# Optimization experiments

Hardware: AMD Instinct MI355X
Metric: run time of the kernel (lower is better)

## Reference

```python
import math
import jax, jax.numpy as jnp
import numpy as np

B, S, E, A, H, L, V = 4, 1024, 1024, 64, 16, 2, 32000
EPS = 1e-5
SCALE = math.sqrt(E)  # torch code scales by sqrt(input_dim) = sqrt(embedding_dim)
W_INIT_SCALE = 0.05   # torch.rand is U[0,1); scaled down for numerically sane softmax


def setup_inputs() -> dict:
    key = jax.random.key(0)
    ks = jax.random.split(key, 6)
    return {
        "x": jax.random.randint(ks[0], (B, S), 0, V),
        "emb": jax.random.normal(ks[1], (V, E), dtype=jnp.float32) * 0.02,
        "ln_gamma": jnp.ones((L, E), dtype=jnp.float32),
        "ln_beta": jnp.zeros((L, E), dtype=jnp.float32),
        "Wq": jax.random.uniform(ks[2], (L, H, A, E), dtype=jnp.float32) * W_INIT_SCALE,
        "Wk": jax.random.uniform(ks[3], (L, H, A, E), dtype=jnp.float32) * W_INIT_SCALE,
        "Wv": jax.random.uniform(ks[4], (L, H, E, E), dtype=jnp.float32) * W_INIT_SCALE,
    }


def _attn_layer(h, gamma, beta, wq, wk, wv):
    # h: [B,H,S,E]; LayerNorm over last dim (biased variance, like torch)
    mu = jnp.mean(h, axis=-1, keepdims=True)
    var = jnp.mean(jnp.square(h - mu), axis=-1, keepdims=True)
    hn = (h - mu) * jax.lax.rsqrt(var + EPS) * gamma + beta
    q = jnp.einsum('bhse,hae->bhsa', hn, wq)   # [B,H,S,A]
    k = jnp.einsum('bhse,hae->bhsa', hn, wk)   # [B,H,S,A]
    v = jnp.einsum('bhse,hoe->bhso', hn, wv)   # [B,H,S,E]
    scores = jnp.einsum('bhsa,bhta->bhst', q, k) / SCALE  # [B,H,S,S]
    w = jax.nn.softmax(scores, axis=-1)
    return jnp.einsum('bhst,bhto->bhso', w, v)  # [B,H,S,E]


def reference(x, emb, ln_gamma, ln_beta, Wq, Wk, Wv):
    # embed then replicate across heads: [B,S,E] -> [B,H,S,E]
    h = jnp.broadcast_to(emb[x][:, None, :, :], (B, H, S, E))
    for l in range(L):
        h = _attn_layer(h, ln_gamma[l], ln_beta[l], Wq[l], Wk[l], Wv[l])
    return h
```

## Files before the change

### kernel.cpp

```cpp
#include <hip/hip_runtime.h>

#define B_ 4
#define S_ 1024
#define E_ 1024
#define A_ 64
#define H_ 16
#define L_ 2

static constexpr float LN_EPS = 1e-5f;
static constexpr float INV_SCALE = 1.0f / 32.0f;

typedef __attribute__((ext_vector_type(8))) short bf16x8;
typedef __attribute__((ext_vector_type(4))) float f32x4;

__device__ __forceinline__ unsigned short f2bf(float f) {
  unsigned u = __float_as_uint(f);
  u += 0x7fffu + ((u >> 16) & 1u);
  return (unsigned short)(u >> 16);
}
__device__ __forceinline__ float bf2f(unsigned short s) {
  return __uint_as_float(((unsigned)s) << 16);
}

__device__ __forceinline__ float block_sum256(float v, float* red) {
#pragma unroll
  for (int o = 32; o > 0; o >>= 1) v += __shfl_down(v, o, 64);
  const int lane = threadIdx.x & 63;
  const int w = threadIdx.x >> 6;
  if (lane == 0) red[w] = v;
  __syncthreads();
  if (threadIdx.x == 0) red[0] = red[0] + red[1] + red[2] + red[3];
  __syncthreads();
  float r = red[0];
  __syncthreads();
  return r;
}

__global__ __launch_bounds__(256) void cvt_f32_bf16(const float* __restrict__ in,
                                                    unsigned short* __restrict__ out, long n) {
  long i = ((long)blockIdx.x * 256 + threadIdx.x) * 4;
  const long stride = (long)gridDim.x * 1024;
  for (; i < n; i += stride) {
    float4 v = *(const float4*)(in + i);
    ushort4 o;
    o.x = f2bf(v.x); o.y = f2bf(v.y); o.z = f2bf(v.z); o.w = f2bf(v.w);
    *(ushort4*)(out + i) = o;
  }
}

__global__ __launch_bounds__(256) void cvt_qk_concat(const float* __restrict__ Wq,
                                                     const float* __restrict__ Wk,
                                                     unsigned short* __restrict__ out) {
  const long total = (long)L_ * H_ * 128 * E_;
  long i = ((long)blockIdx.x * 256 + threadIdx.x) * 4;
  const long stride = (long)gridDim.x * 1024;
  for (; i < total; i += stride) {
    const long e = i % E_;
    const long rowhe = i / E_;
    const int row = (int)(rowhe % 128);
    const long lh = rowhe / 128;
    const float* src = (row < 64 ? Wq : Wk) + (lh * 64 + (row & 63)) * E_ + e;
    float4 v = *(const float4*)src;
    ushort4 o;
    o.x = f2bf(v.x); o.y = f2bf(v.y); o.z = f2bf(v.z); o.w = f2bf(v.w);
    *(ushort4*)(out + i) = o;
  }
}

__global__ __launch_bounds__(256) void embed_ln_kernel(
    const int* __restrict__ x, const float* __restrict__ emb,
    const float* __restrict__ gamma, const float* __restrict__ beta,
    unsigned short* __restrict__ out) {
  __shared__ float red[4];
  const int row = blockIdx.x;
  const int tid = threadIdx.x;
  const float* src = emb + (long)x[row] * E_;
  float4 v = *(const float4*)(src + tid * 4);
  const float mean = block_sum256(v.x + v.y + v.z + v.w, red) * (1.f / E_);
  float dx = v.x - mean, dy = v.y - mean, dz = v.z - mean, dw = v.w - mean;
  const float var = block_sum256(dx * dx + dy * dy + dz * dz + dw * dw, red) * (1.f / E_);
  const float rstd = rsqrtf(var + LN_EPS);
  float4 g = *(const float4*)(gamma + tid * 4);
  float4 b = *(const float4*)(beta + tid * 4);
  ushort4 o;
  o.x = f2bf(dx * rstd * g.x + b.x);
  o.y = f2bf(dy * rstd * g.y + b.y);
  o.z = f2bf(dz * rstd * g.z + b.z);
  o.w = f2bf(dw * rstd * g.w + b.w);
  *(ushort4*)(out + (long)row * E_ + tid * 4) = o;
}

__global__ __launch_bounds__(256) void ln_bf16_kernel(
    const unsigned short* __restrict__ h, const float* __restrict__ gamma,
    const float* __restrict__ beta, unsigned short* __restrict__ out) {
  __shared__ float red[4];
  const long row = blockIdx.x;
  const int tid = threadIdx.x;
  ushort4 raw = *(const ushort4*)(h + row * (long)E_ + tid * 4);
  float vx = bf2f(raw.x), vy = bf2f(raw.y), vz = bf2f(raw.z), vw = bf2f(raw.w);
  const float mean = block_sum256(vx + vy + vz + vw, red) * (1.f / E_);
  float dx = vx - mean, dy = vy - mean, dz = vz - mean, dw = vw - mean;
  const float var = block_sum256(dx * dx + dy * dy + dz * dz + dw * dw, red) * (1.f / E_);
  const float rstd = rsqrtf(var + LN_EPS);
  float4 g = *(const float4*)(gamma + tid * 4);
  float4 b = *(const float4*)(beta + tid * 4);
  ushort4 o;
  o.x = f2bf(dx * rstd * g.x + b.x);
  o.y = f2bf(dy * rstd * g.y + b.y);
  o.z = f2bf(dz * rstd * g.z + b.z);
  o.w = f2bf(dw * rstd * g.w + b.w);
  *(ushort4*)(out + row * E_ + tid * 4) = o;
}

__device__ __forceinline__ void gload_lds16(const void* g, void* l) {
  __builtin_amdgcn_global_load_lds((const __attribute__((address_space(1))) void*)g,
                                   (__attribute__((address_space(3))) void*)l, 16, 0, 0);
}

template <int ROWS>
__device__ __forceinline__ void stage_tile(const unsigned short* __restrict__ src, int ldRow,
                                           unsigned short* lds, int tid) {
  const int rb = tid >> 3;
  const int gslot = (tid & 7) ^ (rb & 7);
  const int wbase = (tid >> 6) * 512;
#pragma unroll
  for (int i = 0; i < ROWS / 32; ++i) {
    const unsigned short* g = src + (long)(i * 32 + rb) * ldRow + gslot * 8;
    gload_lds16(g, lds + i * 2048 + wbase);
  }
}

__device__ __forceinline__ bf16x8 lds_frag(const unsigned short* base, int r, int slot) {
  const int byteoff = (r << 7) + ((slot ^ (r & 7)) << 4);
  return *(const bf16x8*)((const char*)base + byteoff);
}

template <int BM, int BN, bool OUT_BF16>
__global__ __launch_bounds__(256) void mfma_gemm_nt(
    const unsigned short* __restrict__ Aall, const unsigned short* __restrict__ Ball,
    void* __restrict__ Call, int M, int N, int K, int lda, int ldb,
    long aSB, long aSH, long bSB, long bSH, int Hn, float alpha) {
  __shared__ unsigned short As[BM * 64];
  __shared__ unsigned short Bs[BN * 64];
  const int batch = blockIdx.z;
  const int bb = batch / Hn, hh = batch % Hn;
  const unsigned short* Ap = Aall + (long)bb * aSB + (long)hh * aSH;
  const unsigned short* Bp = Ball + (long)bb * bSB + (long)hh * bSH;
  const int tid = threadIdx.x;
  const int lane = tid & 63;
  const int wave = tid >> 6;
  const int wr = wave >> 1, wc = wave & 1;
  const int bm = blockIdx.x * BM, bn = blockIdx.y * BN;
  constexpr int FM = BM / 32, FN = BN / 32;

  f32x4 acc[FM][FN];
#pragma unroll
  for (int i = 0; i < FM; ++i)
#pragma unroll
    for (int j = 0; j < FN; ++j) acc[i][j] = (f32x4)(0.f);

  for (int k0 = 0; k0 < K; k0 += 64) {
    stage_tile<BM>(Ap + (long)bm * lda + k0, lda, As, tid);
    stage_tile<BN>(Bp + (long)bn * ldb + k0, ldb, Bs, tid);
    __syncthreads();
#pragma unroll
    for (int kb = 0; kb < 2; ++kb) {
      const int slot = (kb << 2) + (lane >> 4);
      bf16x8 af[FM], bfv[FN];
#pragma unroll
      for (int mi = 0; mi < FM; ++mi)
        af[mi] = lds_frag(As, wr * (BM / 2) + mi * 16 + (lane & 15), slot);
#pragma unroll
      for (int ni = 0; ni < FN; ++ni)
        bfv[ni] = lds_frag(Bs, wc * (BN / 2) + ni * 16 + (lane & 15), slot);
#pragma unroll
      for (int mi = 0; mi < FM; ++mi)
#pragma unroll
        for (int ni = 0; ni < FN; ++ni)
          acc[mi][ni] = __builtin_amdgcn_mfma_f32_16x16x32_bf16(af[mi], bfv[ni], acc[mi][ni], 0, 0, 0);
    }
    __syncthreads();
  }

#pragma unroll
  for (int mi = 0; mi < FM; ++mi) {
    const int row = bm + wr * (BM / 2) + mi * 16 + ((lane >> 4) << 2);
#pragma unroll
    for (int ni = 0; ni < FN; ++ni) {
      const int col = bn + wc * (BN / 2) + ni * 16 + (lane & 15);
#pragma unroll
      for (int r = 0; r < 4; ++r) {
        const float v = acc[mi][ni][r] * alpha;
        const long idx = (long)batch * M * N + (long)(row + r) * N + col;
        if constexpr (OUT_BF16)
          ((unsigned short*)Call)[idx] = f2bf(v);
        else
          ((float*)Call)[idx] = v;
      }
    }
  }
}

__device__ __forceinline__ void stage_unit256(const unsigned short* __restrict__ src, int ldRow,
                                              char* lds_unit, int tid) {
#pragma unroll
  for (int i = 0; i < 2; ++i) {
    const int r = i * 128 + (tid >> 2);
    const int sg = (tid & 3) ^ ((r >> 1) & 3);
    const unsigned short* g = src + (long)r * ldRow + sg * 8;
    gload_lds16(g, lds_unit + i * 8192 + ((tid >> 6) << 10));
  }
}

__device__ __forceinline__ bf16x8 lds_frag256(const char* opbase, int kh, int r, int ss) {
  return *(const bf16x8*)(opbase + kh * 16384 + r * 64 + ((ss ^ ((r >> 1) & 3)) << 4));
}

template <bool OUT_BF16>
__global__ __launch_bounds__(512, 2) void mfma_gemm256_nt(
    const unsigned short* __restrict__ Aall, const unsigned short* __restrict__ Ball,
    void* __restrict__ Call, int M, int N, int K, int lda, int ldb,
    long aSB, long aSH, long bSB, long bSH, int Hn, float alpha) {
  extern __shared__ char lds[];
  const int nx = gridDim.x, ny = gridDim.y;
  const int nwg = nx * ny * gridDim.z;
  int f = blockIdx.x + nx * (blockIdx.y + ny * blockIdx.z);
  if ((nwg & 7) == 0) f = (f & 7) * (nwg >> 3) + (f >> 3);
  const int bx = f % nx;
  const int by = (f / nx) % ny;
  const int batch = f / (nx * ny);

  const int bb = batch / Hn, hh = batch % Hn;
  const unsigned short* Ap = Aall + (long)bb * aSB + (long)hh * aSH + (long)bx * 256 * lda;
  const unsigned short* Bp = Ball + (long)bb * bSB + (long)hh * bSH + (long)by * 256 * ldb;
  const int tid = threadIdx.x;
  const int lane = tid & 63;
  const int w = tid >> 6;
  const int wr = w >> 2, wc = w & 3;
  const int ss = lane >> 4;
  const int ar = lane & 15;

  f32x4 acc[8][4];
#pragma unroll
  for (int i = 0; i < 8; ++i)
#pragma unroll
    for (int j = 0; j < 4; ++j) acc[i][j] = (f32x4)(0.f);

  const int NT = K >> 6;
  stage_unit256(Ap, lda, lds, tid);
  stage_unit256(Bp, ldb, lds + 32768, tid);
  stage_unit256(Ap + 32, lda, lds + 16384, tid);
  stage_unit256(Bp + 32, ldb, lds + 49152, tid);
  asm volatile("s_waitcnt vmcnt(4)\n\ts_barrier" ::: "memory");

  for (int t = 0; t < NT; ++t) {
    const char* cur = lds + (t & 1) * 65536;
    char* nxt = lds + ((t + 1) & 1) * 65536;
    const unsigned short* An = Ap + (long)(t + 1) * 64;
    const unsigned short* Bn = Bp + (long)(t + 1) * 64;
    const bool pf = (t + 1 < NT);
    bf16x8 a[4], b[4];

#pragma unroll
    for (int ni = 0; ni < 4; ++ni)
      b[ni] = lds_frag256(cur + 32768, 0, wc * 64 + ni * 16 + ar, ss);
#pragma unroll
    for (int mi = 0; mi < 4; ++mi)
      a[mi] = lds_frag256(cur, 0, wr * 128 + mi * 16 + ar, ss);
    if (pf) stage_unit256(An, lda, nxt, tid);
    asm volatile("s_barrier" ::: "memory");
    __builtin_amdgcn_s_setprio(1);
#pragma unroll
    for (int mi = 0; mi < 4; ++mi)
#pragma unroll
      for (int ni = 0; ni < 4; ++ni)
        acc[mi][ni] = __builtin_amdgcn_mfma_f32_16x16x32_bf16(a[mi], b[ni], acc[mi][ni], 0, 0, 0);
    __builtin_amdgcn_s_setprio(0);
    asm volatile("s_barrier" ::: "memory");

#pragma unroll
    for (int mi = 0; mi < 4; ++mi)
      a[mi] = lds_frag256(cur, 0, wr * 128 + 64 + mi * 16 + ar, ss);
    if (pf) stage_unit256(Bn, ldb, nxt + 32768, tid);
    if (pf) asm volatile("s_waitcnt vmcnt(4)\n\ts_barrier" ::: "memory");
    else    asm volatile("s_waitcnt vmcnt(0)\n\ts_barrier" ::: "memory");
    __builtin_amdgcn_s_setprio(1);
#pragma unroll
    for (int mi = 0; mi < 4; ++mi)
#pragma unroll
      for (int ni = 0; ni < 4; ++ni)
        acc[4 + mi][ni] = __builtin_amdgcn_mfma_f32_16x16x32_bf16(a[mi], b[ni], acc[4 + mi][ni], 0, 0, 0);
    __builtin_amdgcn_s_setprio(0);
    asm volatile("s_barrier" ::: "memory");

#pragma unroll
    for (int ni = 0; ni < 4; ++ni)
      b[ni] = lds_frag256(cur + 32768, 1, wc * 64 + ni * 16 + ar, ss);
#pragma unroll
    for (int mi = 0; mi < 4; ++mi)
      a[mi] = lds_frag256(cur, 1, wr * 128 + mi * 16 + ar, ss);
    if (pf) stage_unit256(An + 32, lda, nxt + 16384, tid);
    asm volatile("s_barrier" ::: "memory");
    __builtin_amdgcn_s_setprio(1);
#pragma unroll
    for (int mi = 0; mi < 4; ++mi)
#pragma unroll
      for (int ni = 0; ni < 4; ++ni)
        acc[mi][ni] = __builtin_amdgcn_mfma_f32_16x16x32_bf16(a[mi], b[ni], acc[mi][ni], 0, 0, 0);
    __builtin_amdgcn_s_setprio(0);
    asm volatile("s_barrier" ::: "memory");

#pragma unroll
    for (int mi = 0; mi < 4; ++mi)
      a[mi] = lds_frag256(cur, 1, wr * 128 + 64 + mi * 16 + ar, ss);
    if (pf) {
      stage_unit256(Bn + 32, ldb, nxt + 49152, tid);
      asm volatile("s_waitcnt vmcnt(4)\n\ts_barrier" ::: "memory");
    } else {
      asm volatile("s_barrier" ::: "memory");
    }
    __builtin_amdgcn_s_setprio(1);
#pragma unroll
    for (int mi = 0; mi < 4; ++mi)
#pragma unroll
      for (int ni = 0; ni < 4; ++ni)
        acc[4 + mi][ni] = __builtin_amdgcn_mfma_f32_16x16x32_bf16(a[mi], b[ni], acc[4 + mi][ni], 0, 0, 0);
    __builtin_amdgcn_s_setprio(0);
    asm volatile("s_barrier" ::: "memory");
  }

#pragma unroll
  for (int mi = 0; mi < 8; ++mi) {
    const int row0 = bx * 256 + wr * 128 + mi * 16 + ((lane >> 4) << 2);
#pragma unroll
    for (int ni = 0; ni < 4; ++ni) {
      const int col = by * 256 + wc * 64 + ni * 16 + (lane & 15);
#pragma unroll
      for (int r = 0; r < 4; ++r) {
        const float v = acc[mi][ni][r] * alpha;
        const long idx = (long)batch * M * N + (long)(row0 + r) * N + col;
        if constexpr (OUT_BF16)
          ((unsigned short*)Call)[idx] = f2bf(v);
        else
          ((float*)Call)[idx] = v;
      }
    }
  }
}

__global__ __launch_bounds__(512) void scores_softmax_kernel(
    const unsigned short* __restrict__ qk, unsigned short* __restrict__ sc) {
  extern __shared__ char smem[];
  unsigned short* q_lds = (unsigned short*)smem;
  unsigned short* k_lds = (unsigned short*)(smem + 8192);
  float* redm = (float*)(smem + 8192 + 131072);
  float* reds = redm + 512;

  const int tid = threadIdx.x;
  const int lane = tid & 63;
  const int w = tid >> 6;
  const int batch = blockIdx.z;
  const int bm = blockIdx.x * 64;
  const unsigned short* qbase = qk + (long)batch * S_ * 128 + (long)bm * 128;
  const unsigned short* kbase = qk + (long)batch * S_ * 128 + 64;

  {
    const int r = tid >> 3;
    const int slot = (tid & 7) ^ (r & 7);
    gload_lds16(qbase + (long)r * 128 + slot * 8, (char*)q_lds + w * 1024);
  }
#pragma unroll
  for (int p = 0; p < 16; ++p) {
    const int r = p * 64 + (tid >> 3);
    const int slot = (tid & 7) ^ (r & 7);
    gload_lds16(kbase + (long)r * 128 + slot * 8, (char*)k_lds + p * 8192 + w * 1024);
  }
  __syncthreads();

  const int ss = lane >> 4, ar = lane & 15;
  f32x4 acc[4][8];
#pragma unroll
  for (int i = 0; i < 4; ++i)
#pragma unroll
    for (int j = 0; j < 8; ++j) acc[i][j] = (f32x4)(0.f);

#pragma unroll
  for (int kh = 0; kh < 2; ++kh) {
    bf16x8 a[4];
#pragma unroll
    for (int mi = 0; mi < 4; ++mi)
      a[mi] = lds_frag(q_lds, mi * 16 + ar, kh * 4 + ss);
#pragma unroll
    for (int ni = 0; ni < 8; ++ni) {
      bf16x8 bv = lds_frag(k_lds, w * 128 + ni * 16 + ar, kh * 4 + ss);
#pragma unroll
      for (int mi = 0; mi < 4; ++mi)
        acc[mi][ni] = __builtin_amdgcn_mfma_f32_16x16x32_bf16(a[mi], bv, acc[mi][ni], 0, 0, 0);
    }
  }

#pragma unroll
  for (int mi = 0; mi < 4; ++mi)
#pragma unroll
    for (int ni = 0; ni < 8; ++ni)
#pragma unroll
      for (int r = 0; r < 4; ++r) acc[mi][ni][r] *= INV_SCALE;

  float gmax[4][4];
#pragma unroll
  for (int mi = 0; mi < 4; ++mi)
#pragma unroll
    for (int r = 0; r < 4; ++r) {
      float m = acc[mi][0][r];
#pragma unroll
      for (int ni = 1; ni < 8; ++ni) m = fmaxf(m, acc[mi][ni][r]);
#pragma unroll
      for (int mask = 1; mask < 16; mask <<= 1) m = fmaxf(m, __shfl_xor(m, mask, 64));
      if ((lane & 15) == 0) redm[(mi * 16 + (lane >> 4) * 4 + r) * 8 + w] = m;
      gmax[mi][r] = m;
    }
  __syncthreads();
#pragma unroll
  for (int mi = 0; mi < 4; ++mi)
#pragma unroll
    for (int r = 0; r < 4; ++r) {
      const int row = mi * 16 + (lane >> 4) * 4 + r;
      float g = redm[row * 8];
#pragma unroll
      for (int w2 = 1; w2 < 8; ++w2) g = fmaxf(g, redm[row * 8 + w2]);
      gmax[mi][r] = g;
    }

  float ginv[4][4];
#pragma unroll
  for (int mi = 0; mi < 4; ++mi)
#pragma unroll
    for (int r = 0; r < 4; ++r) {
      float s = 0.f;
#pragma unroll
      for (int ni = 0; ni < 8; ++ni) {
        const float e = __expf(acc[mi][ni][r] - gmax[mi][r]);
        acc[mi][ni][r] = e;
        s += e;
      }
#pragma unroll
      for (int mask = 1; mask < 16; mask <<= 1) s += __shfl_xor(s, mask, 64);
      if ((lane & 15) == 0) reds[(mi * 16 + (lane >> 4) * 4 + r) * 8 + w] = s;
    }
  __syncthreads();
#pragma unroll
  for (int mi = 0; mi < 4; ++mi)
#pragma unroll
    for (int r = 0; r < 4; ++r) {
      const int row = mi * 16 + (lane >> 4) * 4 + r;
      float g = 0.f;
#pragma unroll
      for (int w2 = 0; w2 < 8; ++w2) g += reds[row * 8 + w2];
      ginv[mi][r] = 1.f / g;
    }

  unsigned short* out = sc + (long)batch * S_ * S_;
#pragma unroll
  for (int mi = 0; mi < 4; ++mi)
#pragma unroll
    for (int r = 0; r < 4; ++r) {
      const long row = bm + mi * 16 + (lane >> 4) * 4 + r;
#pragma unroll
      for (int ni = 0; ni < 8; ++ni) {
        const int col = w * 128 + ni * 16 + ar;
        out[row * S_ + col] = f2bf(acc[mi][ni][r] * ginv[mi][r]);
      }
    }
}

extern "C" void kernel_launch(void* const* d_in, const int* in_sizes, int n_in,
                              void* d_out, int out_size, void* d_ws, size_t ws_size,
                              hipStream_t stream) {
  const int* x = (const int*)d_in[0];
  const float* emb = (const float*)d_in[1];
  const float* gamma = (const float*)d_in[2];
  const float* beta = (const float*)d_in[3];
  const float* Wq = (const float*)d_in[4];
  const float* Wk = (const float*)d_in[5];
  const float* Wv = (const float*)d_in[6];
  float* out = (float*)d_out;

  (void)hipFuncSetAttribute(reinterpret_cast<const void*>(&mfma_gemm256_nt<true>),
                            hipFuncAttributeMaxDynamicSharedMemorySize, 131072);
  (void)hipFuncSetAttribute(reinterpret_cast<const void*>(&mfma_gemm256_nt<false>),
                            hipFuncAttributeMaxDynamicSharedMemorySize, 131072);
  (void)hipFuncSetAttribute(reinterpret_cast<const void*>(&scores_softmax_kernel),
                            hipFuncAttributeMaxDynamicSharedMemorySize, 143360);

  const long WQK_N = (long)L_ * H_ * 128 * E_;
  const long WV_N = (long)L_ * H_ * E_ * E_;
  const long HN_N = (long)B_ * H_ * S_ * E_;
  const long QK_N = (long)B_ * H_ * S_ * 128;
  unsigned short* wqk = (unsigned short*)d_ws;
  unsigned short* wv_bf = wqk + WQK_N;
  unsigned short* hn = wv_bf + WV_N;
  unsigned short* qk = hn + HN_N;
  unsigned short* v_t = qk + QK_N;
  unsigned short* sc = v_t + HN_N;
  unsigned short* hid0 = (unsigned short*)d_out;

  const dim3 blk(256), blk512(512);
  const dim3 grid256(4, 4, 64);
  cvt_qk_concat<<<2048, blk, 0, stream>>>(Wq, Wk, wqk);
  cvt_f32_bf16<<<4096, blk, 0, stream>>>(Wv, wv_bf, WV_N);

  for (int l = 0; l < L_; ++l) {
    long hSB, hSH;
    if (l == 0) {
      embed_ln_kernel<<<B_ * S_, blk, 0, stream>>>(x, emb, gamma, beta, hn);
      hSB = (long)S_ * E_; hSH = 0;
    } else {
      ln_bf16_kernel<<<B_ * H_ * S_, blk, 0, stream>>>(
          hid0, gamma + (long)l * E_, beta + (long)l * E_, hn);
      hSB = (long)H_ * S_ * E_; hSH = (long)S_ * E_;
    }
    mfma_gemm_nt<128, 128, true><<<dim3(8, 1, 64), blk, 0, stream>>>(
        hn, wqk + (long)l * H_ * 128 * E_, qk, S_, 128, E_, E_, E_,
        hSB, hSH, 0L, (long)128 * E_, H_, 1.f);
    mfma_gemm256_nt<true><<<grid256, blk512, 131072, stream>>>(
        wv_bf + (long)l * H_ * E_ * E_, hn, v_t, E_, S_, E_, E_, E_,
        0L, (long)E_ * E_, hSB, hSH, H_, 1.f);
    scores_softmax_kernel<<<dim3(16, 1, 64), blk512, 143360, stream>>>(qk, sc);
    if (l == 0) {
      mfma_gemm256_nt<true><<<grid256, blk512, 131072, stream>>>(
          sc, v_t, hid0, S_, E_, S_, S_, S_,
          (long)H_ * S_ * S_, (long)S_ * S_, (long)H_ * E_ * S_, (long)E_ * S_, H_, 1.f);
    } else {
      mfma_gemm256_nt<false><<<grid256, blk512, 131072, stream>>>(
          sc, v_t, out, S_, E_, S_, S_, S_,
          (long)H_ * S_ * S_, (long)S_ * S_, (long)H_ * E_ * S_, (long)E_ * S_, H_, 1.f);
    }
  }
}
```

Baseline: 0.9998 ms.

## Software-pipeline LDS fragment loads across MFMA phases in 256x256 GEMM

Reworks the GEMM main loop so LDS fragment reads for the next phase are issued before the current phase's MFMAs, using separate register sets (a0/a1/bA/bB). The first k-slice's fragments are preloaded before the loop, and the next tile's are loaded at the end of each iteration. B fragments are reused across both M halves. Global stage issue order and waitcnt points are reshuffled to cut the number of barriers. This raises register pressure and the risk of a subtle vmcnt/barrier ordering error.

```diff
diff --git a/kernel.cpp b/kernel.cpp
--- a/kernel.cpp
+++ b/kernel.cpp
@@ -248,10 +248,18 @@
 
   const int NT = K >> 6;
   stage_unit256(Ap, lda, lds, tid);
+  stage_unit256(Ap + 32, lda, lds + 16384, tid);
   stage_unit256(Bp, ldb, lds + 32768, tid);
-  stage_unit256(Ap + 32, lda, lds + 16384, tid);
   stage_unit256(Bp + 32, ldb, lds + 49152, tid);
-  asm volatile("s_waitcnt vmcnt(4)\n\ts_barrier" ::: "memory");
+  asm volatile("s_waitcnt vmcnt(0)\n\ts_barrier" ::: "memory");
+
+  bf16x8 a0[4], a1[4], bA[4], bB[4];
+#pragma unroll
+  for (int ni = 0; ni < 4; ++ni)
+    bA[ni] = lds_frag256(lds + 32768, 0, wc * 64 + ni * 16 + ar, ss);
+#pragma unroll
+  for (int mi = 0; mi < 4; ++mi)
+    a0[mi] = lds_frag256(lds, 0, wr * 128 + mi * 16 + ar, ss);
 
   for (int t = 0; t < NT; ++t) {
     const char* cur = lds + (t & 1) * 65536;
@@ -259,72 +267,67 @@
     const unsigned short* An = Ap + (long)(t + 1) * 64;
     const unsigned short* Bn = Bp + (long)(t + 1) * 64;
     const bool pf = (t + 1 < NT);
-    bf16x8 a[4], b[4];
+
+#pragma unroll
+    for (int mi = 0; mi < 4; ++mi)
+      a1[mi] = lds_frag256(cur, 0, wr * 128 + 64 + mi * 16 + ar, ss);
+    if (pf) {
+      stage_unit256(An, lda, nxt, tid);
+      stage_unit256(Bn, ldb, nxt + 32768, tid);
+    }
+    __builtin_amdgcn_s_setprio(1);
+#pragma unroll
+    for (int mi = 0; mi < 4; ++mi)
+#pragma unroll
+      for (int ni = 0; ni < 4; ++ni)
+        acc[mi][ni] = __builtin_amdgcn_mfma_f32_16x16x32_bf16(a0[mi], bA[ni], acc[mi][ni], 0, 0, 0);
+    __builtin_amdgcn_s_setprio(0);
+    if (pf) asm volatile("s_waitcnt vmcnt(4)\n\ts_barrier" ::: "memory");
+    else    asm volatile("s_waitcnt vmcnt(0)\n\ts_barrier" ::: "memory");
 
 #pragma unroll
     for (int ni = 0; ni < 4; ++ni)
-      b[ni] = lds_frag256(cur + 32768, 0, wc * 64 + ni * 16 + ar, ss);
-#pragma unroll
-    for (int mi = 0; mi < 4; ++mi)
-      a[mi] = lds_frag256(cur, 0, wr * 128 + mi * 16 + ar, ss);
-    if (pf) stage_unit256(An, lda, nxt, tid);
-    asm volatile("s_barrier" ::: "memory");
+      bB[ni] = lds_frag256(cur + 32768, 1, wc * 64 + ni * 16 + ar, ss);
+#pragma unroll
+    for (int mi = 0; mi < 4; ++mi)
+      a0[mi] = lds_frag256(cur, 1, wr * 128 + mi * 16 + ar, ss);
+    if (pf) stage_unit256(An + 32, lda, nxt + 16384, tid);
     __builtin_amdgcn_s_setprio(1);
 #pragma unroll
     for (int mi = 0; mi < 4; ++mi)
 #pragma unroll
       for (int ni = 0; ni < 4; ++ni)
-        acc[mi][ni] = __builtin_amdgcn_mfma_f32_16x16x32_bf16(a[mi], b[ni], acc[mi][ni], 0, 0, 0);
+        acc[4 + mi][ni] = __builtin_amdgcn_mfma_f32_16x16x32_bf16(a1[mi], bA[ni], acc[4 + mi][ni], 0, 0, 0);
     __builtin_amdgcn_s_setprio(0);
     asm volatile("s_barrier" ::: "memory");
 
 #pragma unroll
     for (int mi = 0; mi < 4; ++mi)
-      a[mi] = lds_frag256(cur, 0, wr * 128 + 64 + mi * 16 + ar, ss);
-    if (pf) stage_unit256(Bn, ldb, nxt + 32768, tid);
-    if (pf) asm volatile("s_waitcnt vmcnt(4)\n\ts_barrier" ::: "memory");
-    else    asm volatile("s_waitcnt vmcnt(0)\n\ts_barrier" ::: "memory");
+      a1[mi] = lds_frag256(cur, 1, wr * 128 + 64 + mi * 16 + ar, ss);
+    if (pf) stage_unit256(Bn + 32, ldb, nxt + 49152, tid);
     __builtin_amdgcn_s_setprio(1);
 #pragma unroll
     for (int mi = 0; mi < 4; ++mi)
 #pragma unroll
       for (int ni = 0; ni < 4; ++ni)
-        acc[4 + mi][ni] = __builtin_amdgcn_mfma_f32_16x16x32_bf16(a[mi], b[ni], acc[4 + mi][ni], 0, 0, 0);
+        acc[mi][ni] = __builtin_amdgcn_mfma_f32_16x16x32_bf16(a0[mi], bB[ni], acc[mi][ni], 0, 0, 0);
     __builtin_amdgcn_s_setprio(0);
-    asm volatile("s_barrier" ::: "memory");
-
-#pragma unroll
-    for (int ni = 0; ni < 4; ++ni)
-      b[ni] = lds_frag256(cur + 32768, 1, wc * 64 + ni * 16 + ar, ss);
-#pragma unroll
-    for (int mi = 0; mi < 4; ++mi)
-      a[mi] = lds_frag256(cur, 1, wr * 128 + mi * 16 + ar, ss);
-    if (pf) stage_unit256(An + 32, lda, nxt + 16384, tid);
-    asm volatile("s_barrier" ::: "memory");
+    asm volatile("s_waitcnt vmcnt(4)\n\ts_barrier" ::: "memory");
+
+    if (pf) {
+#pragma unroll
+      for (int ni = 0; ni < 4; ++ni)
+        bA[ni] = lds_frag256(nxt + 32768, 0, wc * 64 + ni * 16 + ar, ss);
+#pragma unroll
+      for (int mi = 0; mi < 4; ++mi)
+        a0[mi] = lds_frag256(nxt, 0, wr * 128 + mi * 16 + ar, ss);
+    }
     __builtin_amdgcn_s_setprio(1);
 #pragma unroll
     for (int mi = 0; mi < 4; ++mi)
 #pragma unroll
       for (int ni = 0; ni < 4; ++ni)
-        acc[mi][ni] = __builtin_amdgcn_mfma_f32_16x16x32_bf16(a[mi], b[ni], acc[mi][ni], 0, 0, 0);
-    __builtin_amdgcn_s_setprio(0);
-    asm volatile("s_barrier" ::: "memory");
-
-#pragma unroll
-    for (int mi = 0; mi < 4; ++mi)
-      a[mi] = lds_frag256(cur, 1, wr * 128 + 64 + mi * 16 + ar, ss);
-    if (pf) {
-      stage_unit256(Bn + 32, ldb, nxt + 49152, tid);
-      asm volatile("s_waitcnt vmcnt(4)\n\ts_barrier" ::: "memory");
-    } else {
-      asm volatile("s_barrier" ::: "memory");
-    }
-    __builtin_amdgcn_s_setprio(1);
-#pragma unroll
-    for (int mi = 0; mi < 4; ++mi)
-#pragma unroll
-      for (int ni = 0; ni < 4; ++ni)
-        acc[4 + mi][ni] = __builtin_amdgcn_mfma_f32_16x16x32_bf16(a[mi], b[ni], acc[4 + mi][ni], 0, 0, 0);
+        acc[4 + mi][ni] = __builtin_amdgcn_mfma_f32_16x16x32_bf16(a1[mi], bB[ni], acc[4 + mi][ni], 0, 0, 0);
     __builtin_amdgcn_s_setprio(0);
     asm volatile("s_barrier" ::: "memory");
   }
```

Result: slower. 1.025 ms (+2.5%).
